# Kernel optimization log

Measured on AMD Instinct MI355X. Metric: run time of the kernel, lower is better.

## Reference

```python
import jax, jax.numpy as jnp
import numpy as np

N = 131072          # number of items ranked in one soft_rank call
CAPACITY = 3.0      # self.capcity in the torch module


def _pav_kl(y, w):
    """KL isotonic regression (non-increasing fit) via Pool-Adjacent-Violators.
    Pooled block value = logsumexp(y_block) - logsumexp(w_block).
    Matches torchsort / fast-soft-sort isotonic_kl. Sequential O(N)."""
    n = y.shape[0]

    def push(i, st):
        ly, lw, val, start, ptr = st
        ly = ly.at[ptr].set(y[i])
        lw = lw.at[ptr].set(w[i])
        val = val.at[ptr].set(y[i] - w[i])
        start = start.at[ptr].set(i)
        ptr = ptr + 1

        def cond(s):
            _, _, v, _, p = s
            return (p >= 2) & (v[p - 2] <= v[p - 1])

        def merge(s):
            ly, lw, v, stt, p = s
            ny = jnp.logaddexp(ly[p - 2], ly[p - 1])
            nw = jnp.logaddexp(lw[p - 2], lw[p - 1])
            return (ly.at[p - 2].set(ny), lw.at[p - 2].set(nw),
                    v.at[p - 2].set(ny - nw), stt, p - 1)

        return jax.lax.while_loop(cond, merge, (ly, lw, val, start, ptr))

    z = jnp.zeros((n,), y.dtype)
    st0 = (z, z, z, jnp.full((n,), n, jnp.int32), jnp.int32(0))
    ly, lw, val, start, ptr = jax.lax.fori_loop(0, n, push, st0)
    # invalidate stale stack slots, then map each element to its block value
    start = jnp.where(jnp.arange(n) < ptr, start, n)
    blk = jnp.searchsorted(start, jnp.arange(n), side='right') - 1
    return val[blk]


@jax.custom_vjp
def isotonic_kl(y, w):
    return _pav_kl(y, w)


def _iso_fwd(y, w):
    sol = _pav_kl(y, w)
    return sol, (y, w, sol)


def _iso_bwd(res, g):
    y, w, sol = res
    n = y.shape[0]
    # blocks = maximal runs of constant solution (exact equality by construction)
    blk = jnp.cumsum(jnp.concatenate([jnp.array([True]), sol[1:] != sol[:-1]])) - 1
    gsum = jax.ops.segment_sum(g, blk, num_segments=n)

    def seg_softmax(v):
        m = jax.ops.segment_max(v, blk, num_segments=n)
        lse = jnp.log(jax.ops.segment_sum(jnp.exp(v - m[blk]), blk, num_segments=n)) + m
        return jnp.exp(v - lse[blk])

    return seg_softmax(y) * gsum[blk], -seg_softmax(w) * gsum[blk]


isotonic_kl.defvjp(_iso_fwd, _iso_bwd)


def soft_rank_kl(scores):
    """torchsort.soft_rank(scores[None], regularization='kl'), strength=1, ascending."""
    n = scores.shape[0]
    w_log = jnp.log(jnp.arange(n, 0, -1, dtype=scores.dtype))  # log([n, ..., 1])
    perm = jnp.argsort(-scores)          # descending, stable
    s = scores[perm]
    sol = isotonic_kl(s, w_log)
    inv = jnp.argsort(perm)
    return jnp.exp(s - sol)[inv]


def setup_inputs() -> dict:
    key = jax.random.key(0)
    k = jax.random.split(key, 5)
    x = jax.random.normal(k[0], (N, 1), jnp.float32)
    # torch Linear default init bounds: 1/sqrt(fan_in)
    w1 = jax.random.uniform(k[1], (1, 32), jnp.float32, -1.0, 1.0)
    b1 = jax.random.uniform(k[2], (32,), jnp.float32, -1.0, 1.0)
    lim2 = 1.0 / np.sqrt(32.0)
    w2 = jax.random.uniform(k[3], (32, 1), jnp.float32, -lim2, lim2)
    b2 = jax.random.uniform(k[4], (1,), jnp.float32, -lim2, lim2)
    return {"x": x, "w1": w1, "b1": b1, "w2": w2, "b2": b2}


def reference(x, w1, b1, w2, b2):
    h = jnp.maximum(x @ w1 + b1, 0.0)            # [N, 32]
    scores = (h @ w2 + b2).reshape(-1)           # [N]
    ranks = soft_rank_kl(scores)                 # [N]
    other = jax.lax.stop_gradient(ranks) % CAPACITY
    ranks = (ranks - other) / CAPACITY + 1.0
    return ranks.reshape(-1, 1)
```

## Files before the change

kernel.cpp:

```cpp
#include <hip/hip_runtime.h>
#include <stdint.h>

typedef unsigned int u32;
typedef unsigned long long u64;

#define N_ITEMS 131072
#define NB 131072
#define NSLICE 4
#define MBLK 64
#define BUCK_PER_BLK 2048
#define CH_PER_BLK 32
#define PAD 65
#define REGSLOT 2048
#define FIXSCALE 268435456.0f
#define FIXMASK ((1ull << 46) - 1)


__device__ __forceinline__ float wsumf(int s, int e) {
  return 0.5f * (float)(e - s + 1) * (float)(2 * N_ITEMS - s - e);
}

__device__ __forceinline__ float key_to_score(u32 key) {
  u32 m = ~key;
  u32 u = (m & 0x80000000u) ? (m ^ 0x80000000u) : ~m;
  return __uint_as_float(u);
}

#define LOG2E 1.4426950408889634f
__device__ __forceinline__ float fexp(float x) { return exp2f(x * LOG2E); }

__device__ __forceinline__ u32 bucket_of(u32 key, u32 kmin, u32 kmax) {
  double scale = (double)NB / ((double)(kmax - kmin) + 1.0);
  u32 b = (u32)((double)(key - kmin) * scale);
  return b < NB ? b : (NB - 1);
}

__device__ __forceinline__ float recSY(int2 r) { return __int_as_float(r.y); }


__global__ void score_key_kernel(const float* __restrict__ x,
                                 const float* __restrict__ w1,
                                 const float* __restrict__ b1,
                                 const float* __restrict__ w2,
                                 const float* __restrict__ b2,
                                 u32* __restrict__ keyRaw,
                                 u32* __restrict__ pmin, u32* __restrict__ pmax,
                                 u64* __restrict__ hist8) {
  __shared__ u32 r0[256], r1[256];
  int t = threadIdx.x;
  int i = blockIdx.x * 256 + t;
#pragma unroll
  for (int k = 0; k < NSLICE; ++k) hist8[(size_t)k * NB + i] = 0ull;
  float xv = x[i];
  float s = b2[0];
#pragma unroll
  for (int j = 0; j < 32; ++j) {
    float h = fmaf(xv, w1[j], b1[j]);
    h = fmaxf(h, 0.0f);
    s = fmaf(h, w2[j], s);
  }
  u32 u = __float_as_uint(s);
  u32 m = u ^ ((u & 0x80000000u) ? 0xFFFFFFFFu : 0x80000000u);
  u32 key = ~m;
  keyRaw[i] = key;
  r0[t] = key; r1[t] = key;
  __syncthreads();
  for (int off = 128; off > 0; off >>= 1) {
    if (t < off) { r0[t] = min(r0[t], r0[t + off]); r1[t] = max(r1[t], r1[t + off]); }
    __syncthreads();
  }
  if (t == 0) { pmin[blockIdx.x] = r0[0]; pmax[blockIdx.x] = r1[0]; }
}


__global__ void hist_kernel(const u32* __restrict__ keyRaw,
                            const u32* __restrict__ pmin, const u32* __restrict__ pmax,
                            u64* __restrict__ hist8, u32* __restrict__ mm) {
  __shared__ u32 s0[256], s1[256];
  int t = threadIdx.x;
  s0[t] = min(pmin[t], pmin[t + 256]);
  s1[t] = max(pmax[t], pmax[t + 256]);
  __syncthreads();
  for (int off = 128; off > 0; off >>= 1) {
    if (t < off) { s0[t] = min(s0[t], s0[t + off]); s1[t] = max(s1[t], s1[t + off]); }
    __syncthreads();
  }
  u32 kmin = s0[0], kmax = s1[0];
  if (blockIdx.x == 0 && t == 0) { mm[0] = kmin; mm[1] = kmax; }
  int i = blockIdx.x * 256 + t;
  u32 key = keyRaw[i];
  u32 g = bucket_of(key, kmin, kmax);
  float smax = key_to_score(kmin);
  float v = fexp(key_to_score(key) - smax);
  u64 fix = (u64)fmaxf(1.0f, fmaf(v, FIXSCALE, 0.5f));
  size_t slice = (size_t)(blockIdx.x & (NSLICE - 1)) * NB;
  atomicAdd(&hist8[slice + g], (1ull << 46) | fix);
}


__global__ __launch_bounds__(256) void scan_pav_merge_kernel(
    const u64* __restrict__ hist8, u64* __restrict__ flags,
    u32* __restrict__ cdf, int2* __restrict__ REC,
    int* __restrict__ cnt2, u32* __restrict__ rstart) {
  __shared__ u32 vals[BUCK_PER_BLK + 1];
  __shared__ float seL[BUCK_PER_BLK];
  __shared__ int   rST[CH_PER_BLK * PAD];
  __shared__ float rSY[CH_PER_BLK * PAD];
  __shared__ u32 sh[256];
  __shared__ u32 red64[64];
  __shared__ int lcnt[CH_PER_BLK];
  __shared__ int ca[16], cb[16], cM[16];
  int t = threadIdx.x, b = blockIdx.x;
  int B0 = b * BUCK_PER_BLK;
  for (int q = 0; q < 8; ++q) {
    int ii = q * 256 + t;
    u64 acc = 0;
#pragma unroll
    for (int c = 0; c < NSLICE; ++c) acc += hist8[(size_t)c * NB + B0 + ii];
    vals[ii] = (u32)(acc >> 46);
    seL[ii] = (float)(acc & FIXMASK) * (1.0f / FIXSCALE);
  }
  __syncthreads();
  u32 loc[8]; u32 s = 0;
  for (int q = 0; q < 8; ++q) { loc[q] = s; s += vals[t * 8 + q]; }
  sh[t] = s;
  __syncthreads();
  for (int off = 1; off < 256; off <<= 1) {
    u32 x2 = (t >= off) ? sh[t - off] : 0u;
    __syncthreads();
    sh[t] += x2;
    __syncthreads();
  }
  if (t == 0) atomicExch(&flags[b], (1ull << 32) | (u64)sh[255]);
  if (t < 64) {
    u32 v = 0;
    if (t < b) {
      u64 f;
      do { f = atomicAdd(&flags[t], 0ull); } while ((u32)(f >> 32) != 1u);
      v = (u32)f;
    }
    red64[t] = v;
  }
  __syncthreads();
  for (int off = 32; off > 0; off >>= 1) {
    if (t < off) red64[t] += red64[t + off];
    __syncthreads();
  }
  u32 exclu = red64[0];
  u32 tbase = ((t == 0) ? 0u : sh[t - 1]) + exclu;
  u32 eb8[8];
  for (int q = 0; q < 8; ++q) { eb8[q] = tbase + loc[q]; vals[t * 8 + q] = eb8[q]; }
  {
    uint4* c4 = (uint4*)(cdf + B0 + t * 8);
    c4[0] = make_uint4(eb8[0], eb8[1], eb8[2], eb8[3]);
    c4[1] = make_uint4(eb8[4], eb8[5], eb8[6], eb8[7]);
  }
  if (t == 255) vals[BUCK_PER_BLK] = exclu + sh[255];
  if (t == 0) rstart[b] = exclu;
  if (b == 0 && t == 0) rstart[MBLK] = N_ITEMS;
  __syncthreads();
  if (t < CH_PER_BLK) {
    int base = t * PAD;
    int ptr = 0; bool have = false;
    float syT = 0.0f; int stT = 0;
    for (int k = 0; k < 64; ++k) {
      u32 cs = vals[t * 64 + k], ce = vals[t * 64 + k + 1];
      if (ce == cs) continue;
      float syC = seL[t * 64 + k];
      int stC = (int)cs, eC = (int)ce - 1;
      while (have) {
        float SWc = wsumf(stC, eC);
        float SWt = wsumf(stT, stC - 1);
        if (!(syT * SWc <= syC * SWt)) break;
        syC += syT; stC = stT;
        if (ptr == 0) { have = false; break; }
        --ptr;
        stT = rST[base + ptr]; syT = rSY[base + ptr];
      }
      if (have) { rST[base + ptr] = stT; rSY[base + ptr] = syT; ++ptr; }
      stT = stC; syT = syC; have = true;
    }
    if (have) { rST[base + ptr] = stT; rSY[base + ptr] = syT; ++ptr; }
    lcnt[t] = ptr;
  }
  __syncthreads();
  for (int j = 0; j < 5; ++j) {
    int P = CH_PER_BLK >> (j + 1);
    if (t < P) {
      int p = t;
      int kL = p << (j + 1), kR = kL + (1 << j);
      int slotL = kL * PAD, slotR = kR * PAD;
      int nL = lcnt[kL], nR = lcnt[kR];
      int a = 0, bb = 0, hasM = 0;
      if (nL > 0 && nR > 0) {
        int gstartR = (int)vals[kR * 64];
        int gendR   = (int)vals[(kR + (1 << j)) * 64];
        float SYL = rSY[slotL + nL - 1]; int stL = rST[slotL + nL - 1];
        float SYR = rSY[slotR];
        int eR = (nR > 1) ? (rST[slotR + 1] - 1) : (gendR - 1);
        float SWL = wsumf(stL, gstartR - 1);
        float SWR = wsumf(gstartR, eR);
        if (SYL * SWR <= SYR * SWL) {
          hasM = 1;
          float SYM = SYL + SYR; int Ms = stL, Me = eR;
          a = 1; bb = 1;
          for (;;) {
            float SWM = wsumf(Ms, Me);
            if (a < nL) {
              float SYe = rSY[slotL + nL - 1 - a]; int ste = rST[slotL + nL - 1 - a];
              float SWe = wsumf(ste, Ms - 1);
              if (SYe * SWM <= SYM * SWe) { SYM += SYe; Ms = ste; ++a; continue; }
            }
            if (bb < nR) {
              float SYb = rSY[slotR + bb]; int sb = rST[slotR + bb];
              int eb = (bb + 1 < nR) ? (rST[slotR + bb + 1] - 1) : (gendR - 1);
              float SWb = wsumf(sb, eb);
              if (SYM * SWb <= SYb * SWM) { SYM += SYb; Me = eb; ++bb; continue; }
            }
            break;
          }
          rST[slotL + nL - a] = Ms; rSY[slotL + nL - a] = SYM;
        }
      }
      ca[p] = a; cb[p] = bb; cM[p] = hasM;
    }
    __syncthreads();
    for (int p = 0; p < P; ++p) {
      int kL = p << (j + 1), kR = kL + (1 << j);
      int nL = lcnt[kL], nR = lcnt[kR];
      int a = ca[p], bb = cb[p], hasM = cM[p];
      int slotL = kL * PAD, slotR = kR * PAD;
      int destBase = slotL + nL - a + hasM;
      int srcBase = slotR + bb;
      int ncopy = nR - bb;
      for (int off = 0; off < ncopy; off += blockDim.x) {
        int k2 = off + t; bool act = k2 < ncopy;
        int vt = 0; float vs = 0.f;
        if (act) { vt = rST[srcBase + k2]; vs = rSY[srcBase + k2]; }
        __syncthreads();
        if (act) { rST[destBase + k2] = vt; rSY[destBase + k2] = vs; }
        __syncthreads();
      }
    }
    __syncthreads();
    if (t < P) {
      int p = t; int kL = p << (j + 1), kR = kL + (1 << j);
      lcnt[kL] = lcnt[kL] - ca[p] + cM[p] + (lcnt[kR] - cb[p]);
    }
    __syncthreads();
  }
  int n = lcnt[0];
  for (int k = t; k < n; k += blockDim.x)
    REC[(size_t)b * REGSLOT + k] = make_int2(rST[k], __float_as_int(rSY[k]));
  if (t == 0) cnt2[b] = n;
}


__device__ void merge3(int2* __restrict__ REC, const u32* __restrict__ rstart,
                       int* lcnt, int* ca, int* cb, int* cM, int baseR, int SR, int t) {
  for (int j = 0; j < 3; ++j) {
    int P = 8 >> (j + 1);
    if (t < P) {
      int p = t;
      int kL = p << (j + 1), kR = kL + (1 << j);
      int slotL = (baseR + kL * SR) * REGSLOT, slotR = (baseR + kR * SR) * REGSLOT;
      int nL = lcnt[kL], nR = lcnt[kR];
      int a = 0, bb = 0, hasM = 0;
      if (nL > 0 && nR > 0) {
        int gstartR = (int)rstart[baseR + kR * SR];
        int gendR   = (int)rstart[baseR + (kR + (1 << j)) * SR];
        int2 rL = REC[slotL + nL - 1];
        float SYL = recSY(rL); int stL = rL.x;
        int2 rR = REC[slotR];
        float SYR = recSY(rR);
        int eR = (nR > 1) ? (REC[slotR + 1].x - 1) : (gendR - 1);
        float SWL = wsumf(stL, gstartR - 1);
        float SWR = wsumf(gstartR, eR);
        if (SYL * SWR <= SYR * SWL) {
          hasM = 1;
          float SYM = SYL + SYR; int Ms = stL, Me = eR;
          a = 1; bb = 1;
          for (;;) {
            float SWM = wsumf(Ms, Me);
            if (a < nL) {
              int2 re = REC[slotL + nL - 1 - a];
              float SYe = recSY(re); int ste = re.x;
              float SWe = wsumf(ste, Ms - 1);
              if (SYe * SWM <= SYM * SWe) { SYM += SYe; Ms = ste; ++a; continue; }
            }
            if (bb < nR) {
              int2 rb = REC[slotR + bb];
              float SYb = recSY(rb); int sb = rb.x;
              int eb = (bb + 1 < nR) ? (REC[slotR + bb + 1].x - 1) : (gendR - 1);
              float SWb = wsumf(sb, eb);
              if (SYM * SWb <= SYb * SWM) { SYM += SYb; Me = eb; ++bb; continue; }
            }
            break;
          }
          REC[slotL + nL - a] = make_int2(Ms, __float_as_int(SYM));
        }
      }
      ca[p] = a; cb[p] = bb; cM[p] = hasM;
    }
    __syncthreads();
    for (int p = 0; p < P; ++p) {
      int kL = p << (j + 1), kR = kL + (1 << j);
      int nL = lcnt[kL], nR = lcnt[kR];
      int a = ca[p], bb = cb[p], hasM = cM[p];
      int slotL = (baseR + kL * SR) * REGSLOT, slotR = (baseR + kR * SR) * REGSLOT;
      int destBase = slotL + nL - a + hasM;
      int srcBase = slotR + bb;
      int ncopy = nR - bb;
      for (int off = 0; off < ncopy; off += (int)blockDim.x) {
        int k2 = off + t; bool act = k2 < ncopy;
        int2 vr = make_int2(0, 0);
        if (act) vr = REC[srcBase + k2];
        __syncthreads();
        if (act) REC[destBase + k2] = vr;
        __syncthreads();
      }
    }
    __syncthreads();
    if (t < P) {
      int p = t; int kL = p << (j + 1), kR = kL + (1 << j);
      lcnt[kL] = lcnt[kL] - ca[p] + cM[p] + (lcnt[kR] - cb[p]);
    }
    __syncthreads();
  }
}

__global__ __launch_bounds__(1024) void merge_all_kernel(int2* __restrict__ REC,
                                                         int* __restrict__ cnt2,
                                                         const u32* __restrict__ rstart,
                                                         u64* __restrict__ done) {
  __shared__ int lcnt[8];
  __shared__ int ca[4], cb[4], cM[4];
  int t = threadIdx.x, b = blockIdx.x;
  int baseR = b * 8;
  if (t < 8) lcnt[t] = cnt2[baseR + t];
  __syncthreads();
  merge3(REC, rstart, lcnt, ca, cb, cM, baseR, 1, t);
  if (t == 0) {
    __threadfence();
    atomicExch(&done[b], (1ull << 32) | (u64)(u32)lcnt[0]);
  }
  if (b != 0) return;
  if (t < 8) {
    u64 f;
    do { f = atomicAdd(&done[t], 0ull); } while ((u32)(f >> 32) != 1u);
    lcnt[t] = (int)(u32)f;
  }
  __threadfence();
  __syncthreads();
  merge3(REC, rstart, lcnt, ca, cb, cM, 0, 8, t);
  if (t == 0) cnt2[0] = lcnt[0];
}


__global__ void out_kernel(const u32* __restrict__ keyRaw, const u32* __restrict__ mm,
                           const u32* __restrict__ cdf,
                           const int2* __restrict__ REC,
                           const int* __restrict__ cnt2, float* __restrict__ out) {
  int i = blockIdx.x * 256 + threadIdx.x;
  u32 key = keyRaw[i];
  u32 kmin = mm[0], kmax = mm[1];
  float smax = key_to_score(kmin);
  u32 g = bucket_of(key, kmin, kmax);
  int p = (int)cdf[g];
  int m = cnt2[0];
  int lo = 0, hi = m - 1;
  while (lo < hi) {
    int mid = (lo + hi + 1) >> 1;
    if (REC[mid].x <= p) lo = mid; else hi = mid - 1;
  }
  int2 r = REC[lo];
  int s0 = r.x;
  int e0 = (lo + 1 < m) ? (REC[lo + 1].x - 1) : (N_ITEMS - 1);
  float SW = wsumf(s0, e0);
  float s = key_to_score(key);
  float rank = fexp(s - smax) * SW / recSY(r);
  out[i] = floorf(rank * (1.0f / 3.0f)) + 1.0f;
}


extern "C" void kernel_launch(void* const* d_in, const int* in_sizes, int n_in,
                              void* d_out, int out_size, void* d_ws, size_t ws_size,
                              hipStream_t stream) {
  const float* x  = (const float*)d_in[0];
  const float* w1 = (const float*)d_in[1];
  const float* b1 = (const float*)d_in[2];
  const float* w2 = (const float*)d_in[3];
  const float* b2 = (const float*)d_in[4];
  float* out = (float*)d_out;

  char* ws = (char*)d_ws;
  size_t o = 0;
  u32* mm     = (u32*)(ws + o); o += 16;
  u32* pmin   = (u32*)(ws + o); o += (size_t)512 * 4;
  u32* pmax   = (u32*)(ws + o); o += (size_t)512 * 4;
  u64* hist8  = (u64*)(ws + o); o += (size_t)NSLICE * NB * 8;
  u64* flags  = (u64*)(ws + o); o += (size_t)MBLK * 8;
  u64* done   = (u64*)(ws + o); o += (size_t)16 * 8;
  u32* cdf    = (u32*)(ws + o); o += (size_t)(NB + 4) * 4;
  u32* rstart = (u32*)(ws + o); o += (size_t)(MBLK + 4) * 4;
  u32* keyRaw = (u32*)(ws + o); o += (size_t)N_ITEMS * 4;
  int2* REC   = (int2*)(ws + o); o += (size_t)N_ITEMS * 8;
  int* cnt2   = (int*)(ws + o);  o += (size_t)MBLK * 4;

  score_key_kernel<<<512, 256, 0, stream>>>(x, w1, b1, w2, b2,
                                            keyRaw, pmin, pmax, hist8);
  hist_kernel<<<512, 256, 0, stream>>>(keyRaw, pmin, pmax, hist8, mm);
  scan_pav_merge_kernel<<<MBLK, 256, 0, stream>>>(hist8, flags, cdf, REC, cnt2, rstart);
  merge_all_kernel<<<8, 1024, 0, stream>>>(REC, cnt2, rstart, done);
  out_kernel<<<512, 256, 0, stream>>>(keyRaw, mm, cdf, REC, cnt2, out);
}
```

Baseline: 115.5 us.

## Parallelize block-list copy across merge pairs and halve histogram slices

The post-merge copy step used to loop over merge pairs one at a time, each with barrier-separated rounds. Now all pairs are handled at once, with the thread block split into P groups, and the redundant barrier after the copy is dropped. NSLICE is cut from 4 to 2, which halves the partial-histogram slices that get summed, but it may raise atomic contention per slice. In the LDS merge the copy now runs a fixed 4 rounds, which assumes each segment has at most 4*G2 entries. That could silently truncate larger lists.

```diff
diff --git a/kernel.cpp b/kernel.cpp
--- a/kernel.cpp
+++ b/kernel.cpp
@@ -6,7 +6,7 @@
 
 #define N_ITEMS 131072
 #define NB 131072
-#define NSLICE 4
+#define NSLICE 2
 #define MBLK 64
 #define BUCK_PER_BLK 2048
 #define CH_PER_BLK 32
@@ -14,6 +14,7 @@
 #define REGSLOT 2048
 #define FIXSCALE 268435456.0f
 #define FIXMASK ((1ull << 46) - 1)
+#define TAG (1ull << 32)
 
 
 __device__ __forceinline__ float wsumf(int s, int e) {
@@ -131,7 +132,7 @@
     sh[t] += x2;
     __syncthreads();
   }
-  if (t == 0) atomicExch(&flags[b], (1ull << 32) | (u64)sh[255]);
+  if (t == 0) atomicExch(&flags[b], TAG | (u64)sh[255]);
   if (t < 64) {
     u32 v = 0;
     if (t < b) {
@@ -225,16 +226,19 @@
       ca[p] = a; cb[p] = bb; cM[p] = hasM;
     }
     __syncthreads();
-    for (int p = 0; p < P; ++p) {
-      int kL = p << (j + 1), kR = kL + (1 << j);
-      int nL = lcnt[kL], nR = lcnt[kR];
-      int a = ca[p], bb = cb[p], hasM = cM[p];
-      int slotL = kL * PAD, slotR = kR * PAD;
-      int destBase = slotL + nL - a + hasM;
-      int srcBase = slotR + bb;
-      int ncopy = nR - bb;
-      for (int off = 0; off < ncopy; off += blockDim.x) {
-        int k2 = off + t; bool act = k2 < ncopy;
+    {
+      int G2 = 256 / P;
+      int p = t / G2, tl = t - p * G2;
+      int destBase = 0, srcBase = 0, ncopy = 0;
+      if (p < P) {
+        int kL = p << (j + 1), kR = kL + (1 << j);
+        destBase = kL * PAD + lcnt[kL] - ca[p] + cM[p];
+        srcBase  = kR * PAD + cb[p];
+        ncopy    = lcnt[kR] - cb[p];
+      }
+      for (int r = 0; r < 4; ++r) {
+        int k2 = r * G2 + tl;
+        bool act = (p < P) && (k2 < ncopy);
         int vt = 0; float vs = 0.f;
         if (act) { vt = rST[srcBase + k2]; vs = rSY[srcBase + k2]; }
         __syncthreads();
@@ -242,7 +246,6 @@
         __syncthreads();
       }
     }
-    __syncthreads();
     if (t < P) {
       int p = t; int kL = p << (j + 1), kR = kL + (1 << j);
       lcnt[kL] = lcnt[kL] - ca[p] + cM[p] + (lcnt[kR] - cb[p]);
@@ -257,7 +260,8 @@
 
 
 __device__ void merge3(int2* __restrict__ REC, const u32* __restrict__ rstart,
-                       int* lcnt, int* ca, int* cb, int* cM, int baseR, int SR, int t) {
+                       int* lcnt, int* ca, int* cb, int* cM, int* nc,
+                       int baseR, int SR, int t) {
   for (int j = 0; j < 3; ++j) {
     int P = 8 >> (j + 1);
     if (t < P) {
@@ -301,18 +305,26 @@
         }
       }
       ca[p] = a; cb[p] = bb; cM[p] = hasM;
-    }
-    __syncthreads();
-    for (int p = 0; p < P; ++p) {
-      int kL = p << (j + 1), kR = kL + (1 << j);
-      int nL = lcnt[kL], nR = lcnt[kR];
-      int a = ca[p], bb = cb[p], hasM = cM[p];
-      int slotL = (baseR + kL * SR) * REGSLOT, slotR = (baseR + kR * SR) * REGSLOT;
-      int destBase = slotL + nL - a + hasM;
-      int srcBase = slotR + bb;
-      int ncopy = nR - bb;
-      for (int off = 0; off < ncopy; off += (int)blockDim.x) {
-        int k2 = off + t; bool act = k2 < ncopy;
+      nc[p] = lcnt[kR] - bb;
+    }
+    __syncthreads();
+    {
+      int B = (int)blockDim.x;
+      int G2 = B / P;
+      int p = t / G2, tl = t - p * G2;
+      int destBase = 0, srcBase = 0, ncopy = 0;
+      if (p < P) {
+        int kL = p << (j + 1), kR = kL + (1 << j);
+        destBase = (baseR + kL * SR) * REGSLOT + lcnt[kL] - ca[p] + cM[p];
+        srcBase  = (baseR + kR * SR) * REGSLOT + cb[p];
+        ncopy    = nc[p];
+      }
+      int mx = 0;
+      for (int i2 = 0; i2 < P; ++i2) mx = max(mx, nc[i2]);
+      int rounds = (mx + G2 - 1) / G2;
+      for (int r = 0; r < rounds; ++r) {
+        int k2 = r * G2 + tl;
+        bool act = (p < P) && (k2 < ncopy);
         int2 vr = make_int2(0, 0);
         if (act) vr = REC[srcBase + k2];
         __syncthreads();
@@ -320,7 +332,6 @@
         __syncthreads();
       }
     }
-    __syncthreads();
     if (t < P) {
       int p = t; int kL = p << (j + 1), kR = kL + (1 << j);
       lcnt[kL] = lcnt[kL] - ca[p] + cM[p] + (lcnt[kR] - cb[p]);
@@ -334,15 +345,15 @@
                                                          const u32* __restrict__ rstart,
                                                          u64* __restrict__ done) {
   __shared__ int lcnt[8];
-  __shared__ int ca[4], cb[4], cM[4];
+  __shared__ int ca[4], cb[4], cM[4], nc[4];
   int t = threadIdx.x, b = blockIdx.x;
   int baseR = b * 8;
   if (t < 8) lcnt[t] = cnt2[baseR + t];
   __syncthreads();
-  merge3(REC, rstart, lcnt, ca, cb, cM, baseR, 1, t);
+  merge3(REC, rstart, lcnt, ca, cb, cM, nc, baseR, 1, t);
   if (t == 0) {
     __threadfence();
-    atomicExch(&done[b], (1ull << 32) | (u64)(u32)lcnt[0]);
+    atomicExch(&done[b], TAG | (u64)(u32)lcnt[0]);
   }
   if (b != 0) return;
   if (t < 8) {
@@ -352,7 +363,7 @@
   }
   __threadfence();
   __syncthreads();
-  merge3(REC, rstart, lcnt, ca, cb, cM, 0, 8, t);
+  merge3(REC, rstart, lcnt, ca, cb, cM, nc, 0, 8, t);
   if (t == 0) cnt2[0] = lcnt[0];
 }
 
```

After: 123.6 us. 6.9% more time.
